# Kernel tuning notes

Measured on AMD Instinct MI355X. Metric: run time of the kernel, lower is better.

## Reference

```python
import jax, jax.numpy as jnp
import numpy as np

N_NODES = 50000
N_EDGES = 800000
IN_CH, HID, OUT_CH, HEADS = 128, 32, 32, 8
NEG_SLOPE = 0.2


def setup_inputs() -> dict:
    key = jax.random.key(0)
    ks = jax.random.split(key, 20)
    x = jax.random.normal(ks[0], (N_NODES, IN_CH), dtype=jnp.float32)
    edge_index = jax.random.randint(ks[1], (2, N_EDGES), 0, N_NODES, dtype=jnp.int64)
    s = 0.1
    # encoder layer 1: in -> hid, heads=8 (concat)
    W1 = jax.random.normal(ks[2], (IN_CH, HEADS * HID), jnp.float32) * s
    as1 = jax.random.normal(ks[3], (HEADS, HID), jnp.float32) * s
    ad1 = jax.random.normal(ks[4], (HEADS, HID), jnp.float32) * s
    b1 = jnp.zeros((HEADS * HID,), jnp.float32)
    # encoder layer 2: hid*heads -> out, heads=1
    W2 = jax.random.normal(ks[5], (HEADS * HID, OUT_CH), jnp.float32) * s
    as2 = jax.random.normal(ks[6], (1, OUT_CH), jnp.float32) * s
    ad2 = jax.random.normal(ks[7], (1, OUT_CH), jnp.float32) * s
    b2 = jnp.zeros((OUT_CH,), jnp.float32)
    # decoder layer 1: out -> hid, heads=8 (concat)
    W3 = jax.random.normal(ks[8], (OUT_CH, HEADS * HID), jnp.float32) * s
    as3 = jax.random.normal(ks[9], (HEADS, HID), jnp.float32) * s
    ad3 = jax.random.normal(ks[10], (HEADS, HID), jnp.float32) * s
    b3 = jnp.zeros((HEADS * HID,), jnp.float32)
    # decoder layer 2: hid*heads -> in, heads=1
    W4 = jax.random.normal(ks[11], (HEADS * HID, IN_CH), jnp.float32) * s
    as4 = jax.random.normal(ks[12], (1, IN_CH), jnp.float32) * s
    ad4 = jax.random.normal(ks[13], (1, IN_CH), jnp.float32) * s
    b4 = jnp.zeros((IN_CH,), jnp.float32)
    return dict(x=x, edge_index=edge_index, W1=W1, as1=as1, ad1=ad1, b1=b1,
                W2=W2, as2=as2, ad2=ad2, b2=b2, W3=W3, as3=as3, ad3=ad3, b3=b3,
                W4=W4, as4=as4, ad4=ad4, b4=b4)


def gat_conv(x, src, dst, W, a_src, a_dst, b, heads, ch):
    # PyG GATConv: h = xW, e_ij = LeakyReLU(a_src.h_j + a_dst.h_i), softmax over incoming edges of i
    h = (x @ W).reshape(-1, heads, ch)                       # [N, H, C]
    al_s = jnp.sum(h * a_src[None], axis=-1)                 # [N, H]
    al_d = jnp.sum(h * a_dst[None], axis=-1)                 # [N, H]
    e = jax.nn.leaky_relu(al_s[src] + al_d[dst], NEG_SLOPE)  # [E, H]
    emax = jax.ops.segment_max(e, dst, num_segments=N_NODES)
    ee = jnp.exp(e - emax[dst])
    denom = jax.ops.segment_sum(ee, dst, num_segments=N_NODES)
    alpha = ee / denom[dst]                                  # [E, H]
    msg = alpha[:, :, None] * h[src]                         # [E, H, C]
    out = jax.ops.segment_sum(msg, dst, num_segments=N_NODES)  # [N, H, C]
    return out.reshape(N_NODES, heads * ch) + b


def reference(x, edge_index, W1, as1, ad1, b1, W2, as2, ad2, b2,
              W3, as3, ad3, b3, W4, as4, ad4, b4):
    # add self loops (PyG default add_self_loops=True)
    loop = jnp.arange(N_NODES, dtype=edge_index.dtype)
    src = jnp.concatenate([edge_index[0], loop])
    dst = jnp.concatenate([edge_index[1], loop])
    # encode
    z = gat_conv(x, src, dst, W1, as1, ad1, b1, HEADS, HID)
    z = jax.nn.relu(z)
    z = gat_conv(z, src, dst, W2, as2, ad2, b2, 1, OUT_CH)
    # decode
    r = gat_conv(z, src, dst, W3, as3, ad3, b3, HEADS, HID)
    r = jax.nn.relu(r)
    r = gat_conv(r, src, dst, W4, as4, ad4, b4, 1, IN_CH)
    return r
```

## Files before the change

### kernel.cpp

```cpp
#include <hip/hip_runtime.h>
#include <math.h>

#define N_NODES 50000
#define N_EDGES 800000
#define N_TOT   850000
#define NSB     ((N_NODES + 255) / 256)

typedef __attribute__((ext_vector_type(8))) short short8;
typedef __attribute__((ext_vector_type(4))) float floatx4;

__device__ __forceinline__ unsigned int pack_bf16x2(float a, float b) {
    unsigned ua = __float_as_uint(a);
    unsigned ub = __float_as_uint(b);
    ua += 0x7fff + ((ua >> 16) & 1);
    ub += 0x7fff + ((ub >> 16) & 1);
    return (ua >> 16) | (ub & 0xffff0000u);
}
__device__ __forceinline__ unsigned short pack_bf16(float a) {
    unsigned ua = __float_as_uint(a);
    ua += 0x7fff + ((ua >> 16) & 1);
    return (unsigned short)(ua >> 16);
}
__device__ __forceinline__ float bf16_lo(unsigned u) { return __uint_as_float(u << 16); }
__device__ __forceinline__ float bf16_hi(unsigned u) { return __uint_as_float(u & 0xffff0000u); }

__global__ void zero_int_kernel(int* p, int n) {
    int i = blockIdx.x * blockDim.x + threadIdx.x;
    if (i < n) p[i] = 0;
}

__global__ void deg_hist_kernel(const int* __restrict__ ei, int* __restrict__ deg) {
    int e = blockIdx.x * blockDim.x + threadIdx.x;
    if (e >= N_TOT) return;
    int dst = (e < N_EDGES) ? ei[N_EDGES + e] : (e - N_EDGES);
    atomicAdd(&deg[dst], 1);
}

__global__ void block_scan_kernel(const int* __restrict__ deg, int* __restrict__ part,
                                  int* __restrict__ bsum) {
    __shared__ int tmp[256];
    int t = threadIdx.x;
    int i = blockIdx.x * 256 + t;
    int v = (i < N_NODES) ? deg[i] : 0;
    tmp[t] = v;
    __syncthreads();
    for (int d = 1; d < 256; d <<= 1) {
        int u = (t >= d) ? tmp[t - d] : 0;
        __syncthreads();
        tmp[t] += u;
        __syncthreads();
    }
    if (i < N_NODES) part[i] = tmp[t] - v;
    if (t == 255) bsum[blockIdx.x] = tmp[255];
}

__global__ void scan_bsum_kernel(int* __restrict__ bsum) {
    __shared__ int tmp[256];
    int t = threadIdx.x;
    int v = (t < NSB) ? bsum[t] : 0;
    tmp[t] = v;
    __syncthreads();
    for (int d = 1; d < 256; d <<= 1) {
        int u = (t >= d) ? tmp[t - d] : 0;
        __syncthreads();
        tmp[t] += u;
        __syncthreads();
    }
    if (t < NSB) bsum[t] = tmp[t] - v;
}

__global__ void finalize_off_kernel(const int* __restrict__ part, const int* __restrict__ bsum,
                                    int* __restrict__ off, int* __restrict__ cursor) {
    int i = blockIdx.x * 256 + threadIdx.x;
    if (i < N_NODES) {
        int o = part[i] + bsum[blockIdx.x];
        off[i] = o;
        cursor[i] = o;
    }
    if (i == 0) off[N_NODES] = N_TOT;
}

__global__ void fill_csr_kernel(const int* __restrict__ ei, int* __restrict__ cursor,
                                int* __restrict__ csr_src) {
    int e = blockIdx.x * blockDim.x + threadIdx.x;
    if (e >= N_TOT) return;
    int src, dst;
    if (e < N_EDGES) { src = ei[e]; dst = ei[N_EDGES + e]; }
    else             { src = dst = e - N_EDGES; }
    int pos = atomicAdd(&cursor[dst], 1);
    csr_src[pos] = src;
}

__global__ void wconv_kernel(const float* __restrict__ W1, const float* __restrict__ W2,
                             const float* __restrict__ W3, const float* __restrict__ W4,
                             unsigned short* __restrict__ T1, unsigned short* __restrict__ T2,
                             unsigned short* __restrict__ T3, unsigned short* __restrict__ T4) {
    int i = blockIdx.x * 256 + threadIdx.x;
    const float* W; unsigned short* T; int K, N, idx;
    if      (i < 32768) { W = W1; T = T1; K = 128; N = 256; idx = i; }
    else if (i < 40960) { W = W2; T = T2; K = 256; N = 32;  idx = i - 32768; }
    else if (i < 49152) { W = W3; T = T3; K = 32;  N = 256; idx = i - 40960; }
    else if (i < 81920) { W = W4; T = T4; K = 256; N = 128; idx = i - 49152; }
    else return;
    int n = idx / K, k = idx % K;
    T[idx] = pack_bf16(W[(size_t)k * N + n]);
}

template<int Cin, int Cout, int H, int C, int NPB, int NW_N, bool IN_BF16>
__global__ void gemm_mfma_kernel(const void* __restrict__ xin,
                                 const unsigned short* __restrict__ Wt,
                                 const float* __restrict__ a_src, const float* __restrict__ a_dst,
                                 unsigned short* __restrict__ hb,
                                 float* __restrict__ al_s, float* __restrict__ al_d) {
    constexpr int NW_M = 4 / NW_N;
    constexpr int MT_W = (NPB / 16) / NW_M;
    constexpr int NT_W = (Cout / 16) / NW_N;
    constexpr int AS   = Cin + 8;
    constexpr int SP   = Cout + 4;
    __shared__ unsigned short xs[NPB * AS];
    __shared__ float hs[NPB * SP];
    int tid = threadIdx.x;
    int n0  = blockIdx.x * NPB;

    if (IN_BF16) {
        for (int i = tid; i < NPB * Cin / 8; i += 256) {
            int n = i / (Cin / 8), k8 = i % (Cin / 8);
            uint4 q = make_uint4(0u, 0u, 0u, 0u);
            if (n0 + n < N_NODES)
                q = ((const uint4*)((const unsigned short*)xin + (size_t)(n0 + n) * Cin))[k8];
            *(uint4*)(xs + n * AS + k8 * 8) = q;
        }
    } else {
        for (int i = tid; i < NPB * Cin / 4; i += 256) {
            int n = i / (Cin / 4), k4 = i % (Cin / 4);
            float4 v = make_float4(0.f, 0.f, 0.f, 0.f);
            if (n0 + n < N_NODES)
                v = ((const float4*)((const float*)xin + (size_t)(n0 + n) * Cin))[k4];
            uint2 p;
            p.x = pack_bf16x2(v.x, v.y);
            p.y = pack_bf16x2(v.z, v.w);
            *(uint2*)(xs + n * AS + k4 * 4) = p;
        }
    }
    __syncthreads();

    int w = tid >> 6, lane = tid & 63;
    int q = lane >> 4, l16 = lane & 15;
    int wm = w / NW_N, wn = w % NW_N;
    int mbase = wm * MT_W * 16;
    int nbase = wn * NT_W * 16;

    floatx4 acc[MT_W][NT_W];
#pragma unroll
    for (int mt = 0; mt < MT_W; mt++)
#pragma unroll
        for (int nt = 0; nt < NT_W; nt++) acc[mt][nt] = (floatx4){0.f, 0.f, 0.f, 0.f};

#pragma unroll
    for (int k0 = 0; k0 < Cin; k0 += 32) {
        short8 a[MT_W], b[NT_W];
#pragma unroll
        for (int mt = 0; mt < MT_W; mt++)
            a[mt] = *(const short8*)(xs + (mbase + mt * 16 + l16) * AS + k0 + q * 8);
#pragma unroll
        for (int nt = 0; nt < NT_W; nt++)
            b[nt] = *(const short8*)(Wt + (size_t)(nbase + nt * 16 + l16) * Cin + k0 + q * 8);
#pragma unroll
        for (int mt = 0; mt < MT_W; mt++)
#pragma unroll
            for (int nt = 0; nt < NT_W; nt++)
                acc[mt][nt] = __builtin_amdgcn_mfma_f32_16x16x32_bf16(a[mt], b[nt], acc[mt][nt], 0, 0, 0);
    }

#pragma unroll
    for (int mt = 0; mt < MT_W; mt++)
#pragma unroll
        for (int nt = 0; nt < NT_W; nt++)
#pragma unroll
            for (int r = 0; r < 4; r++) {
                int nl = mbase + mt * 16 + q * 4 + r;
                int ch = nbase + nt * 16 + l16;
                hs[nl * SP + ch] = acc[mt][nt][r];
            }
    __syncthreads();

    constexpr int TPN = Cout / 32;
    constexpr int TPH = (C > 32) ? (C / 32) : 1;
    if (tid < NPB * TPN) {
        int node = tid / TPN, sub = tid % TPN;
        int gn = n0 + node;
        int head = (sub * 32) / C;
        int coff = (sub * 32) % C;
        const float* hrow = hs + node * SP + sub * 32;
        const float* ap = a_src + head * C + coff;
        const float* dp = a_dst + head * C + coff;
        float ps = 0.f, pd = 0.f;
#pragma unroll
        for (int c4 = 0; c4 < 8; c4++) {
            float4 hv = *(const float4*)(hrow + c4 * 4);
            float4 av = *(const float4*)(ap + c4 * 4);
            float4 dv = *(const float4*)(dp + c4 * 4);
            ps += hv.x * av.x + hv.y * av.y + hv.z * av.z + hv.w * av.w;
            pd += hv.x * dv.x + hv.y * dv.y + hv.z * dv.z + hv.w * dv.w;
        }
        uint4 o0, o1;
        {
            float4 h0 = *(const float4*)(hrow + 0);
            float4 h1 = *(const float4*)(hrow + 4);
            float4 h2 = *(const float4*)(hrow + 8);
            float4 h3 = *(const float4*)(hrow + 12);
            o0.x = pack_bf16x2(h0.x, h0.y); o0.y = pack_bf16x2(h0.z, h0.w);
            o0.z = pack_bf16x2(h1.x, h1.y); o0.w = pack_bf16x2(h1.z, h1.w);
            o1.x = pack_bf16x2(h2.x, h2.y); o1.y = pack_bf16x2(h2.z, h2.w);
            o1.z = pack_bf16x2(h3.x, h3.y); o1.w = pack_bf16x2(h3.z, h3.w);
        }
        uint4 o2, o3;
        {
            float4 h0 = *(const float4*)(hrow + 16);
            float4 h1 = *(const float4*)(hrow + 20);
            float4 h2 = *(const float4*)(hrow + 24);
            float4 h3 = *(const float4*)(hrow + 28);
            o2.x = pack_bf16x2(h0.x, h0.y); o2.y = pack_bf16x2(h0.z, h0.w);
            o2.z = pack_bf16x2(h1.x, h1.y); o2.w = pack_bf16x2(h1.z, h1.w);
            o3.x = pack_bf16x2(h2.x, h2.y); o3.y = pack_bf16x2(h2.z, h2.w);
            o3.z = pack_bf16x2(h3.x, h3.y); o3.w = pack_bf16x2(h3.z, h3.w);
        }
        if (gn < N_NODES) {
            uint4* dst4 = (uint4*)(hb + ((size_t)sub * N_NODES + gn) * 32);
            dst4[0] = o0; dst4[1] = o1; dst4[2] = o2; dst4[3] = o3;
        }
        if (TPH > 1) {
#pragma unroll
            for (int k = 1; k < TPH; k <<= 1) {
                ps += __shfl_xor(ps, k, 64);
                pd += __shfl_xor(pd, k, 64);
            }
            if ((sub % TPH) == 0 && gn < N_NODES) {
                al_s[(size_t)head * N_NODES + gn] = ps;
                al_d[(size_t)head * N_NODES + gn] = pd;
            }
        } else {
            if (gn < N_NODES) {
                al_s[(size_t)head * N_NODES + gn] = ps;
                al_d[(size_t)head * N_NODES + gn] = pd;
            }
        }
    }
}

template<int H, int C, int NP, bool RELU, bool OUT_BF16>
__launch_bounds__(256, 8)
__global__ void gat_agg_kernel(const unsigned short* __restrict__ hb,
                               const float* __restrict__ al_s,
                               const float* __restrict__ al_d,
                               const int* __restrict__ off,
                               const int* __restrict__ csr_src,
                               const float* __restrict__ bias,
                               void* __restrict__ out) {
    constexpr int HC = H * C;
    const int p   = blockIdx.x % NP;
    const int nch = blockIdx.x / NP;
    int tid  = threadIdx.x;
    int lane = tid & 63;
    int wid  = tid >> 6;
    int gi   = lane >> 3;
    int g    = lane & 7;
    int node = nch * 32 + wid * 8 + gi;
    if (node >= N_NODES) return;

    const int head = (H > 1) ? p : 0;
    const float* __restrict__ als_p = al_s + (size_t)head * N_NODES;
    const uint2* __restrict__ hbp   = (const uint2*)hb + (size_t)p * N_NODES * 8;
    int nb = lane & 56;

    int r0 = off[node], r1 = off[node + 1];
    float ald = al_d[(size_t)head * N_NODES + node];

    float4 acc = make_float4(0.f, 0.f, 0.f, 0.f);
    float wsum = 0.f;

    int j0 = r0;
    int idx0 = j0 + g;
    int sC = csr_src[(idx0 < r1) ? idx0 : (r1 - 1)];
    float eC = als_p[sC] + ald;

    for (; j0 + 8 <= r1; j0 += 8) {
        int idxn = j0 + 8 + g;
        int sN = csr_src[(idxn < r1) ? idxn : (r1 - 1)];
        float eL = fmaxf(eC, 0.2f * eC);
        float wC = __expf(eL);
        float eN = als_p[sN] + ald;
#pragma unroll
        for (int u = 0; u < 8; u++) {
            float wu = __shfl(wC, nb + u, 64);
            int   su = __shfl(sC, nb + u, 64);
            uint2 q = hbp[(size_t)su * 8 + g];
            wsum += wu;
            acc.x += wu * bf16_lo(q.x); acc.y += wu * bf16_hi(q.x);
            acc.z += wu * bf16_lo(q.y); acc.w += wu * bf16_hi(q.y);
        }
        sC = sN; eC = eN;
    }
    if (j0 < r1) {
        bool valid = (j0 + g) < r1;
        float eL = fmaxf(eC, 0.2f * eC);
        float wC = valid ? __expf(eL) : 0.f;
#pragma unroll
        for (int u = 0; u < 8; u++) {
            float wu = __shfl(wC, nb + u, 64);
            if (wu != 0.f) {
                int su = __shfl(sC, nb + u, 64);
                uint2 q = hbp[(size_t)su * 8 + g];
                wsum += wu;
                acc.x += wu * bf16_lo(q.x); acc.y += wu * bf16_hi(q.x);
                acc.z += wu * bf16_lo(q.y); acc.w += wu * bf16_hi(q.y);
            }
        }
    }

    float inv = 1.f / wsum;
    float4 bv = ((const float4*)bias)[p * 8 + g];
    acc.x = acc.x * inv + bv.x;
    acc.y = acc.y * inv + bv.y;
    acc.z = acc.z * inv + bv.z;
    acc.w = acc.w * inv + bv.w;
    if (RELU) {
        acc.x = fmaxf(acc.x, 0.f); acc.y = fmaxf(acc.y, 0.f);
        acc.z = fmaxf(acc.z, 0.f); acc.w = fmaxf(acc.w, 0.f);
    }
    size_t oidx = (size_t)node * (HC / 4) + p * 8 + g;
    if (OUT_BF16) {
        uint2 pk;
        pk.x = pack_bf16x2(acc.x, acc.y);
        pk.y = pack_bf16x2(acc.z, acc.w);
        ((uint2*)out)[oidx] = pk;
    } else {
        ((float4*)out)[oidx] = acc;
    }
}

extern "C" void kernel_launch(void* const* d_in, const int* in_sizes, int n_in,
                              void* d_out, int out_size, void* d_ws, size_t ws_size,
                              hipStream_t stream) {
    const float* x   = (const float*)d_in[0];
    const int*   ei  = (const int*)d_in[1];
    const float* W1  = (const float*)d_in[2];
    const float* as1 = (const float*)d_in[3];
    const float* ad1 = (const float*)d_in[4];
    const float* b1  = (const float*)d_in[5];
    const float* W2  = (const float*)d_in[6];
    const float* as2 = (const float*)d_in[7];
    const float* ad2 = (const float*)d_in[8];
    const float* b2  = (const float*)d_in[9];
    const float* W3  = (const float*)d_in[10];
    const float* as3 = (const float*)d_in[11];
    const float* ad3 = (const float*)d_in[12];
    const float* b3  = (const float*)d_in[13];
    const float* W4  = (const float*)d_in[14];
    const float* as4 = (const float*)d_in[15];
    const float* ad4 = (const float*)d_in[16];
    const float* b4  = (const float*)d_in[17];

    char* ws = (char*)d_ws;
    size_t o = 0;
    auto alloc = [&](size_t bytes) -> void* {
        void* p = ws + o;
        o = (o + bytes + 255) & ~(size_t)255;
        return p;
    };
    unsigned short* feat_a  = (unsigned short*)alloc((size_t)N_NODES * 256 * 2);
    unsigned short* feat_b  = (unsigned short*)alloc((size_t)N_NODES * 32 * 2);
    unsigned short* h_buf   = (unsigned short*)alloc((size_t)N_NODES * 256 * 2);
    float*          al_s    = (float*)alloc((size_t)N_NODES * 8 * 4);
    float*          al_d    = (float*)alloc((size_t)N_NODES * 8 * 4);
    int*            deg     = (int*)alloc((size_t)(N_NODES + 1) * 4);
    int*            off     = (int*)alloc((size_t)(N_NODES + 1) * 4);
    int*            cursor  = (int*)alloc((size_t)N_NODES * 4);
    int*            part    = (int*)alloc((size_t)N_NODES * 4);
    int*            bsum    = (int*)alloc((size_t)256 * 4);
    int*            csr_src = (int*)alloc((size_t)N_TOT * 4);
    unsigned short* w1t     = (unsigned short*)alloc(32768 * 2);
    unsigned short* w2t     = (unsigned short*)alloc(8192 * 2);
    unsigned short* w3t     = (unsigned short*)alloc(8192 * 2);
    unsigned short* w4t     = (unsigned short*)alloc(32768 * 2);

    const int TPB = 256;
    int nb_nodes = (N_NODES + TPB - 1) / TPB;
    int nb_edges = (N_TOT + TPB - 1) / TPB;

    zero_int_kernel<<<nb_nodes, TPB, 0, stream>>>(deg, N_NODES);
    wconv_kernel<<<320, TPB, 0, stream>>>(W1, W2, W3, W4, w1t, w2t, w3t, w4t);
    deg_hist_kernel<<<nb_edges, TPB, 0, stream>>>(ei, deg);
    block_scan_kernel<<<NSB, TPB, 0, stream>>>(deg, part, bsum);
    scan_bsum_kernel<<<1, TPB, 0, stream>>>(bsum);
    finalize_off_kernel<<<NSB, TPB, 0, stream>>>(part, bsum, off, cursor);
    fill_csr_kernel<<<nb_edges, TPB, 0, stream>>>(ei, cursor, csr_src);

    const int NBC = (N_NODES + 31) / 32;

    gemm_mfma_kernel<128, 256, 8, 32, 32, 4, false>
        <<<(N_NODES + 31) / 32, TPB, 0, stream>>>(x, w1t, as1, ad1, h_buf, al_s, al_d);
    gat_agg_kernel<8, 32, 8, true, true>
        <<<8 * NBC, TPB, 0, stream>>>(h_buf, al_s, al_d, off, csr_src, b1, feat_a);

    gemm_mfma_kernel<256, 32, 1, 32, 64, 2, true>
        <<<(N_NODES + 63) / 64, TPB, 0, stream>>>(feat_a, w2t, as2, ad2, h_buf, al_s, al_d);
    gat_agg_kernel<1, 32, 1, false, true>
        <<<NBC, TPB, 0, stream>>>(h_buf, al_s, al_d, off, csr_src, b2, feat_b);

    gemm_mfma_kernel<32, 256, 8, 32, 32, 4, true>
        <<<(N_NODES + 31) / 32, TPB, 0, stream>>>(feat_b, w3t, as3, ad3, h_buf, al_s, al_d);
    gat_agg_kernel<8, 32, 8, true, true>
        <<<8 * NBC, TPB, 0, stream>>>(h_buf, al_s, al_d, off, csr_src, b3, feat_a);

    gemm_mfma_kernel<256, 128, 1, 128, 32, 4, true>
        <<<(N_NODES + 31) / 32, TPB, 0, stream>>>(feat_a, w4t, as4, ad4, h_buf, al_s, al_d);
    gat_agg_kernel<1, 128, 4, false, false>
        <<<4 * NBC, TPB, 0, stream>>>(h_buf, al_s, al_d, off, csr_src, b4, d_out);
}
```

Baseline: 519.0 us.

## Assign one wavefront per node in GAT aggregation with cross-lane reduction

The aggregation kernel changes from one 8-lane group per node to one 64-lane wavefront per node. Each of the 8 lane groups handles a strided subset of edges, and partial sums are combined with xor-shuffles before one group writes the output. This removes the per-edge shuffle broadcast and gives each high-degree node more parallel gather work. The cost is 8x more blocks, a reduction tree per node, and idle lanes for nodes with fewer than 8 edges (average degree is about 17).

```diff
diff --git a/kernel.cpp b/kernel.cpp
--- a/kernel.cpp
+++ b/kernel.cpp
@@ -263,15 +263,14 @@
     int tid  = threadIdx.x;
     int lane = tid & 63;
     int wid  = tid >> 6;
-    int gi   = lane >> 3;
+    int e    = lane >> 3;
     int g    = lane & 7;
-    int node = nch * 32 + wid * 8 + gi;
+    int node = nch * 4 + wid;
     if (node >= N_NODES) return;
 
     const int head = (H > 1) ? p : 0;
     const float* __restrict__ als_p = al_s + (size_t)head * N_NODES;
     const uint2* __restrict__ hbp   = (const uint2*)hb + (size_t)p * N_NODES * 8;
-    int nb = lane & 56;
 
     int r0 = off[node], r1 = off[node + 1];
     float ald = al_d[(size_t)head * N_NODES + node];
@@ -279,63 +278,56 @@
     float4 acc = make_float4(0.f, 0.f, 0.f, 0.f);
     float wsum = 0.f;
 
-    int j0 = r0;
-    int idx0 = j0 + g;
-    int sC = csr_src[(idx0 < r1) ? idx0 : (r1 - 1)];
+    int j0  = r0;
+    int idx = r0 + e;
+    int   sC = csr_src[(idx < r1) ? idx : (r1 - 1)];
+    bool  vC = idx < r1;
     float eC = als_p[sC] + ald;
 
-    for (; j0 + 8 <= r1; j0 += 8) {
-        int idxn = j0 + 8 + g;
-        int sN = csr_src[(idxn < r1) ? idxn : (r1 - 1)];
+    for (;;) {
+        int jn   = j0 + 8;
+        int idxn = jn + e;
+        int   sN = csr_src[(idxn < r1) ? idxn : (r1 - 1)];
+        float eN = als_p[sN] + ald;
         float eL = fmaxf(eC, 0.2f * eC);
-        float wC = __expf(eL);
-        float eN = als_p[sN] + ald;
-#pragma unroll
-        for (int u = 0; u < 8; u++) {
-            float wu = __shfl(wC, nb + u, 64);
-            int   su = __shfl(sC, nb + u, 64);
-            uint2 q = hbp[(size_t)su * 8 + g];
-            wsum += wu;
-            acc.x += wu * bf16_lo(q.x); acc.y += wu * bf16_hi(q.x);
-            acc.z += wu * bf16_lo(q.y); acc.w += wu * bf16_hi(q.y);
-        }
-        sC = sN; eC = eN;
-    }
-    if (j0 < r1) {
-        bool valid = (j0 + g) < r1;
-        float eL = fmaxf(eC, 0.2f * eC);
-        float wC = valid ? __expf(eL) : 0.f;
-#pragma unroll
-        for (int u = 0; u < 8; u++) {
-            float wu = __shfl(wC, nb + u, 64);
-            if (wu != 0.f) {
-                int su = __shfl(sC, nb + u, 64);
-                uint2 q = hbp[(size_t)su * 8 + g];
-                wsum += wu;
-                acc.x += wu * bf16_lo(q.x); acc.y += wu * bf16_hi(q.x);
-                acc.z += wu * bf16_lo(q.y); acc.w += wu * bf16_hi(q.y);
-            }
-        }
-    }
-
-    float inv = 1.f / wsum;
-    float4 bv = ((const float4*)bias)[p * 8 + g];
-    acc.x = acc.x * inv + bv.x;
-    acc.y = acc.y * inv + bv.y;
-    acc.z = acc.z * inv + bv.z;
-    acc.w = acc.w * inv + bv.w;
-    if (RELU) {
-        acc.x = fmaxf(acc.x, 0.f); acc.y = fmaxf(acc.y, 0.f);
-        acc.z = fmaxf(acc.z, 0.f); acc.w = fmaxf(acc.w, 0.f);
-    }
-    size_t oidx = (size_t)node * (HC / 4) + p * 8 + g;
-    if (OUT_BF16) {
-        uint2 pk;
-        pk.x = pack_bf16x2(acc.x, acc.y);
-        pk.y = pack_bf16x2(acc.z, acc.w);
-        ((uint2*)out)[oidx] = pk;
-    } else {
-        ((float4*)out)[oidx] = acc;
+        float w  = vC ? __expf(eL) : 0.f;
+        uint2 q  = hbp[(size_t)sC * 8 + g];
+        wsum  += w;
+        acc.x += w * bf16_lo(q.x); acc.y += w * bf16_hi(q.x);
+        acc.z += w * bf16_lo(q.y); acc.w += w * bf16_hi(q.y);
+        if (jn >= r1) break;
+        j0 = jn; sC = sN; eC = eN; vC = idxn < r1;
+    }
+
+#pragma unroll
+    for (int m = 8; m < 64; m <<= 1) {
+        wsum  += __shfl_xor(wsum, m, 64);
+        acc.x += __shfl_xor(acc.x, m, 64);
+        acc.y += __shfl_xor(acc.y, m, 64);
+        acc.z += __shfl_xor(acc.z, m, 64);
+        acc.w += __shfl_xor(acc.w, m, 64);
+    }
+
+    if (e == 0) {
+        float inv = 1.f / wsum;
+        float4 bv = ((const float4*)bias)[p * 8 + g];
+        acc.x = acc.x * inv + bv.x;
+        acc.y = acc.y * inv + bv.y;
+        acc.z = acc.z * inv + bv.z;
+        acc.w = acc.w * inv + bv.w;
+        if (RELU) {
+            acc.x = fmaxf(acc.x, 0.f); acc.y = fmaxf(acc.y, 0.f);
+            acc.z = fmaxf(acc.z, 0.f); acc.w = fmaxf(acc.w, 0.f);
+        }
+        size_t oidx = (size_t)node * (HC / 4) + p * 8 + g;
+        if (OUT_BF16) {
+            uint2 pk;
+            pk.x = pack_bf16x2(acc.x, acc.y);
+            pk.y = pack_bf16x2(acc.z, acc.w);
+            ((uint2*)out)[oidx] = pk;
+        } else {
+            ((float4*)out)[oidx] = acc;
+        }
     }
 }
 
@@ -396,25 +388,25 @@
     finalize_off_kernel<<<NSB, TPB, 0, stream>>>(part, bsum, off, cursor);
     fill_csr_kernel<<<nb_edges, TPB, 0, stream>>>(ei, cursor, csr_src);
 
-    const int NBC = (N_NODES + 31) / 32;
+    const int NBW = (N_NODES + 3) / 4;
 
     gemm_mfma_kernel<128, 256, 8, 32, 32, 4, false>
         <<<(N_NODES + 31) / 32, TPB, 0, stream>>>(x, w1t, as1, ad1, h_buf, al_s, al_d);
     gat_agg_kernel<8, 32, 8, true, true>
-        <<<8 * NBC, TPB, 0, stream>>>(h_buf, al_s, al_d, off, csr_src, b1, feat_a);
+        <<<8 * NBW, TPB, 0, stream>>>(h_buf, al_s, al_d, off, csr_src, b1, feat_a);
 
     gemm_mfma_kernel<256, 32, 1, 32, 64, 2, true>
         <<<(N_NODES + 63) / 64, TPB, 0, stream>>>(feat_a, w2t, as2, ad2, h_buf, al_s, al_d);
     gat_agg_kernel<1, 32, 1, false, true>
-        <<<NBC, TPB, 0, stream>>>(h_buf, al_s, al_d, off, csr_src, b2, feat_b);
+        <<<NBW, TPB, 0, stream>>>(h_buf, al_s, al_d, off, csr_src, b2, feat_b);
 
     gemm_mfma_kernel<32, 256, 8, 32, 32, 4, true>
         <<<(N_NODES + 31) / 32, TPB, 0, stream>>>(feat_b, w3t, as3, ad3, h_buf, al_s, al_d);
     gat_agg_kernel<8, 32, 8, true, true>
-        <<<8 * NBC, TPB, 0, stream>>>(h_buf, al_s, al_d, off, csr_src, b3, feat_a);
+        <<<8 * NBW, TPB, 0, stream>>>(h_buf, al_s, al_d, off, csr_src, b3, feat_a);
 
     gemm_mfma_kernel<256, 128, 1, 128, 32, 4, true>
         <<<(N_NODES + 31) / 32, TPB, 0, stream>>>(feat_a, w4t, as4, ad4, h_buf, al_s, al_d);
     gat_agg_kernel<1, 128, 4, false, false>
-        <<<4 * NBC, TPB, 0, stream>>>(h_buf, al_s, al_d, off, csr_src, b4, d_out);
-}
+        <<<4 * NBW, TPB, 0, stream>>>(h_buf, al_s, al_d, off, csr_src, b4, d_out);
+}
```

After: 683.1 us. +31.6%, slower.

## Sort nodes by in-degree bucket to balance aggregation warps

Applied to the files above, without the earlier changes.

Builds a counting-sort permutation of nodes by in-degree (clamped at 255) using three small new kernels, then has each aggregation thread group process nodes in that permuted order. Nodes with similar degree share a wavefront, so divergence from uneven edge-loop trip counts is reduced. The cost is extra small launches and scattered, non-coalesced output writes and per-node metadata reads, since neighbouring lanes now handle unrelated node ids.

```diff
diff --git a/kernel.cpp b/kernel.cpp
--- a/kernel.cpp
+++ b/kernel.cpp
@@ -104,6 +104,37 @@
     else return;
     int n = idx / K, k = idx % K;
     T[idx] = pack_bf16(W[(size_t)k * N + n]);
+}
+
+__global__ void deg_bucket_kernel(const int* __restrict__ deg, int* __restrict__ hist) {
+    int i = blockIdx.x * 256 + threadIdx.x;
+    if (i < N_NODES) {
+        int d = deg[i]; if (d > 255) d = 255;
+        atomicAdd(&hist[d], 1);
+    }
+}
+__global__ void scan_hist_kernel(int* __restrict__ hist) {
+    __shared__ int tmp[256];
+    int t = threadIdx.x;
+    int v = hist[t];
+    tmp[t] = v;
+    __syncthreads();
+    for (int d = 1; d < 256; d <<= 1) {
+        int u = (t >= d) ? tmp[t - d] : 0;
+        __syncthreads();
+        tmp[t] += u;
+        __syncthreads();
+    }
+    hist[t] = tmp[t] - v;
+}
+__global__ void scatter_perm_kernel(const int* __restrict__ deg, int* __restrict__ hist,
+                                    int* __restrict__ perm) {
+    int i = blockIdx.x * 256 + threadIdx.x;
+    if (i < N_NODES) {
+        int d = deg[i]; if (d > 255) d = 255;
+        int pos = atomicAdd(&hist[d], 1);
+        perm[pos] = i;
+    }
 }
 
 template<int Cin, int Cout, int H, int C, int NPB, int NW_N, bool IN_BF16>
@@ -255,6 +286,7 @@
                                const float* __restrict__ al_d,
                                const int* __restrict__ off,
                                const int* __restrict__ csr_src,
+                               const int* __restrict__ perm,
                                const float* __restrict__ bias,
                                void* __restrict__ out) {
     constexpr int HC = H * C;
@@ -265,8 +297,9 @@
     int wid  = tid >> 6;
     int gi   = lane >> 3;
     int g    = lane & 7;
-    int node = nch * 32 + wid * 8 + gi;
-    if (node >= N_NODES) return;
+    int ni   = nch * 32 + wid * 8 + gi;
+    if (ni >= N_NODES) return;
+    int node = perm[ni];
 
     const int head = (H > 1) ? p : 0;
     const float* __restrict__ als_p = al_s + (size_t)head * N_NODES;
@@ -379,6 +412,8 @@
     int*            part    = (int*)alloc((size_t)N_NODES * 4);
     int*            bsum    = (int*)alloc((size_t)256 * 4);
     int*            csr_src = (int*)alloc((size_t)N_TOT * 4);
+    int*            hist    = (int*)alloc((size_t)256 * 4);
+    int*            perm    = (int*)alloc((size_t)N_NODES * 4);
     unsigned short* w1t     = (unsigned short*)alloc(32768 * 2);
     unsigned short* w2t     = (unsigned short*)alloc(8192 * 2);
     unsigned short* w3t     = (unsigned short*)alloc(8192 * 2);
@@ -389,8 +424,12 @@
     int nb_edges = (N_TOT + TPB - 1) / TPB;
 
     zero_int_kernel<<<nb_nodes, TPB, 0, stream>>>(deg, N_NODES);
+    zero_int_kernel<<<1, TPB, 0, stream>>>(hist, 256);
     wconv_kernel<<<320, TPB, 0, stream>>>(W1, W2, W3, W4, w1t, w2t, w3t, w4t);
     deg_hist_kernel<<<nb_edges, TPB, 0, stream>>>(ei, deg);
+    deg_bucket_kernel<<<NSB, TPB, 0, stream>>>(deg, hist);
+    scan_hist_kernel<<<1, TPB, 0, stream>>>(hist);
+    scatter_perm_kernel<<<NSB, TPB, 0, stream>>>(deg, hist, perm);
     block_scan_kernel<<<NSB, TPB, 0, stream>>>(deg, part, bsum);
     scan_bsum_kernel<<<1, TPB, 0, stream>>>(bsum);
     finalize_off_kernel<<<NSB, TPB, 0, stream>>>(part, bsum, off, cursor);
@@ -401,20 +440,20 @@
     gemm_mfma_kernel<128, 256, 8, 32, 32, 4, false>
         <<<(N_NODES + 31) / 32, TPB, 0, stream>>>(x, w1t, as1, ad1, h_buf, al_s, al_d);
     gat_agg_kernel<8, 32, 8, true, true>
-        <<<8 * NBC, TPB, 0, stream>>>(h_buf, al_s, al_d, off, csr_src, b1, feat_a);
+        <<<8 * NBC, TPB, 0, stream>>>(h_buf, al_s, al_d, off, csr_src, perm, b1, feat_a);
 
     gemm_mfma_kernel<256, 32, 1, 32, 64, 2, true>
         <<<(N_NODES + 63) / 64, TPB, 0, stream>>>(feat_a, w2t, as2, ad2, h_buf, al_s, al_d);
     gat_agg_kernel<1, 32, 1, false, true>
-        <<<NBC, TPB, 0, stream>>>(h_buf, al_s, al_d, off, csr_src, b2, feat_b);
+        <<<NBC, TPB, 0, stream>>>(h_buf, al_s, al_d, off, csr_src, perm, b2, feat_b);
 
     gemm_mfma_kernel<32, 256, 8, 32, 32, 4, true>
         <<<(N_NODES + 31) / 32, TPB, 0, stream>>>(feat_b, w3t, as3, ad3, h_buf, al_s, al_d);
     gat_agg_kernel<8, 32, 8, true, true>
-        <<<8 * NBC, TPB, 0, stream>>>(h_buf, al_s, al_d, off, csr_src, b3, feat_a);
+        <<<8 * NBC, TPB, 0, stream>>>(h_buf, al_s, al_d, off, csr_src, perm, b3, feat_a);
 
     gemm_mfma_kernel<256, 128, 1, 128, 32, 4, true>
         <<<(N_NODES + 31) / 32, TPB, 0, stream>>>(feat_a, w4t, as4, ad4, h_buf, al_s, al_d);
     gat_agg_kernel<1, 128, 4, false, false>
-        <<<4 * NBC, TPB, 0, stream>>>(h_buf, al_s, al_d, off, csr_src, b4, d_out);
-}
+        <<<4 * NBC, TPB, 0, stream>>>(h_buf, al_s, al_d, off, csr_src, perm, b4, d_out);
+}
```

Result: slower. 823.2 us (+58.6%).
